# Performance work log

Hardware: AMD Instinct MI355X
Metric: run time of the kernel (lower is better)

## Reference

```python
import jax, jax.numpy as jnp
import numpy as np
from jax import lax

B, T, N, L, C, K = 8, 168, 512, 4, 32, 50

def setup_inputs() -> dict:
    key = jax.random.key(0)
    ks = iter(jax.random.split(key, 40))
    rn = lambda *s: jax.random.normal(next(ks), s, dtype=jnp.float32)
    inp = {}
    inp['input'] = rn(B, 7, T, N)
    inp['missing_nodes'] = jax.random.randint(next(ks), (B, K), 0, N)
    # two provided supports: random row-normalized adjacency
    a0 = jax.random.uniform(next(ks), (N, N)); inp['sup0'] = a0 / a0.sum(1, keepdims=True)
    a1 = jax.random.uniform(next(ks), (N, N)); inp['sup1'] = a1 / a1.sum(1, keepdims=True)
    inp['nodevec1'] = rn(N, 10); inp['nodevec2'] = rn(10, N)
    s = 0.05
    inp['skip_w'] = rn(C, 4) * s; inp['skip_b'] = jnp.zeros((C,))
    inp['filter_w'] = rn(L, C, C, 2) * s; inp['filter_b'] = jnp.zeros((L, C))
    inp['gate_w'] = rn(L, C, C, 2) * s; inp['gate_b'] = jnp.zeros((L, C))
    inp['gconv_w'] = rn(L, C, 7 * C) * s; inp['gconv_b'] = jnp.zeros((L, C))  # (2*3+1)*32=224
    inp['ingru_w'] = rn(1, C) * s; inp['ingru_b'] = jnp.zeros((1,))
    inp['regru_w'] = rn(C, 1) * s; inp['regru_b'] = jnp.zeros((C,))
    inp['zl_w'] = rn(N, 2 * N) * s; inp['zl_b'] = jnp.zeros((N,))
    inp['rl_w'] = rn(N, 2 * N) * s; inp['rl_b'] = jnp.zeros((N,))
    inp['hl_w'] = rn(N, 2 * N) * s; inp['hl_b'] = jnp.zeros((N,))
    inp['end1_w'] = rn(64, C) * s; inp['end1_b'] = jnp.zeros((64,))
    inp['end2_w'] = rn(1, 64) * s; inp['end2_b'] = jnp.zeros((1,))
    return inp

def _conv1x1(x, w, b):  # x (B,Cin,N,T), w (Cout,Cin)
    return jnp.einsum('bcnt,oc->bont', x, w) + b[None, :, None, None]

def _conv1x2(x, w, b):  # x (B,Cin,N,T+1), w (Cout,Cin,2) -> (B,Cout,N,T)
    return (jnp.einsum('bcnt,oc->bont', x[..., :-1], w[..., 0])
            + jnp.einsum('bcnt,oc->bont', x[..., 1:], w[..., 1])
            + b[None, :, None, None])

def _gcn(x, supports, w, b):  # Graph WaveNet gcn, order=2, eval mode (no dropout)
    outs = [x]
    for a in supports:
        x1 = jnp.einsum('bcnt,nm->bcmt', x, a)
        outs.append(x1)
        outs.append(jnp.einsum('bcnt,nm->bcmt', x1, a))
    return _conv1x1(jnp.concatenate(outs, axis=1), w, b)

def reference(input, missing_nodes, sup0, sup1, nodevec1, nodevec2,
              skip_w, skip_b, filter_w, filter_b, gate_w, gate_b,
              gconv_w, gconv_b, ingru_w, ingru_b, regru_w, regru_b,
              zl_w, zl_b, rl_w, rl_b, hl_w, hl_b,
              end1_w, end1_b, end2_w, end2_b):
    M = input[:, 1]                                   # (B,T,N) missingness mask
    x = jnp.transpose(input[:, jnp.array([0, 3, 5, 6])], (0, 1, 3, 2))  # (B,4,N,T)
    x = _conv1x1(x, skip_w, skip_b)                   # (B,32,N,T)
    adp = jax.nn.softmax(jax.nn.relu(nodevec1 @ nodevec2), axis=1)
    supports = [sup0, sup1, adp]
    Mt = jnp.transpose(M, (1, 0, 2))                  # (T,B,N)

    def cell(h, xm):
        Xi, Mi = xm
        xin = jax.nn.sigmoid(Xi * Mi + h * (1.0 - Mi))
        xh = jnp.concatenate([xin, h], axis=1)        # (B,2N)
        z = jax.nn.sigmoid(xh @ zl_w.T + zl_b)
        r = jax.nn.sigmoid(xh @ rl_w.T + rl_b)
        cr = jnp.concatenate([xin, r * h], axis=1)
        h_t = jnp.tanh(cr @ hl_w.T + hl_b)
        h = (1.0 - z) * h + z * h_t
        return h, h

    skip = None
    for i in range(L):
        xp = jnp.pad(x, ((0, 0), (0, 0), (0, 0), (1, 0)))    # pad time left
        residual = xp
        f = jnp.tanh(_conv1x2(xp, filter_w[i], filter_b[i]))
        g = jax.nn.sigmoid(_conv1x2(xp, gate_w[i], gate_b[i]))
        xg = f * g                                           # (B,32,N,T)
        skip = xg if skip is None else xg + skip
        gout = _gcn(xg, supports, gconv_w[i], gconv_b[i])    # (B,32,N,T); gnn == gconv output (eval)
        X = _conv1x1(gout, ingru_w, ingru_b)[:, 0]           # (B,N,T)
        Xt = jnp.transpose(X, (2, 0, 1))                     # (T,B,N)
        h0 = jnp.zeros((input.shape[0], X.shape[1]), dtype=x.dtype)
        _, outs = lax.scan(cell, h0, (Xt, Mt))               # (T,B,N)
        outputs = jnp.transpose(outs, (1, 0, 2))             # (B,T,N)
        re = _conv1x1(outputs[:, None], regru_w, regru_b)    # (B,32,T,N)
        re = jnp.transpose(re, (0, 1, 3, 2))                 # (B,32,N,T)
        x = re + residual[..., -f.shape[3]:] + gout

    h = jax.nn.relu(skip)
    h = jax.nn.relu(_conv1x1(h, end1_w, end1_b))
    h = _conv1x1(h, end2_w, end2_b)[:, 0]                    # (B,N,T)
    idx = jnp.broadcast_to(missing_nodes[:, :, None], (h.shape[0], missing_nodes.shape[1], h.shape[2]))
    return jnp.take_along_axis(h, idx, axis=1)               # (B,K,T)
```

## Files before the change

### kernel.cpp

```cpp
#include <hip/hip_runtime.h>
#include <math.h>

#define Bb 8
#define Tt 168
#define Nn 512
#define Cc 32
#define Ll 4
#define Kk 50
#define NCH 4
#define BPC 2
#define BTc (BPC*Tt)
#define BTNc ((size_t)BTc*Nn)
#define BTCNc ((size_t)BTc*Cc*Nn)
#define BT (Bb*Tt)
#define BTN ((size_t)Bb*Tt*Nn)
#define BTCN ((size_t)Bb*Tt*Cc*Nn)
#define GRUB 64

typedef __attribute__((ext_vector_type(8))) short short8v;
typedef __attribute__((ext_vector_type(4))) float f32x4;
typedef __attribute__((ext_vector_type(2))) float f32x2;

__device__ __forceinline__ float sigm(float v) { return 1.0f/(1.0f + expf(-v)); }

__device__ __forceinline__ unsigned int f2bf(float x) {
  unsigned int u = __float_as_uint(x);
  u = u + 0x7FFFu + ((u >> 16) & 1u);
  return u >> 16;
}
__device__ __forceinline__ float bf2f(unsigned int h) {
  return __uint_as_float(h << 16);
}

__device__ __forceinline__ void sysstore(float* p, float v) {
  __hip_atomic_store(p, v, __ATOMIC_RELAXED, __HIP_MEMORY_SCOPE_SYSTEM);
}
__device__ __forceinline__ int flagload(const int* p) {
  return __hip_atomic_load(p, __ATOMIC_RELAXED, __HIP_MEMORY_SCOPE_AGENT);
}
__device__ __forceinline__ void flagstore(int* p, int v) {
  __hip_atomic_store(p, v, __ATOMIC_RELAXED, __HIP_MEMORY_SCOPE_AGENT);
}

__device__ __forceinline__ void byp_store4(float* p, f32x4 v) {
  asm volatile("global_store_dwordx4 %0, %1, off sc0 sc1" :: "v"(p), "v"(v) : "memory");
}

__global__ void k_wt2(const float* __restrict__ zl, const float* __restrict__ rl,
                      const float* __restrict__ hl, float* __restrict__ wpack) {
  int idx = blockIdx.x*256 + threadIdx.x;
  if (idx >= GRUB*8*3072) return;
  int kk = idx % 3072;
  int c  = (idx / 3072) & 7;
  int sl = idx / (3072*8);
  int ncol = sl*8 + c;
  float v;
  if (kk < 1024)      v = zl[ncol*1024 + kk];
  else if (kk < 2048) v = rl[ncol*1024 + (kk-1024)];
  else if (kk < 2560) v = hl[ncol*1024 + (kk-2048)];
  else                v = hl[ncol*1024 + 512 + (kk-2560)];
  wpack[idx] = v;
}

__global__ void k_adp(const float* __restrict__ nv1, const float* __restrict__ nv2,
                      float* __restrict__ adp) {
  int i = blockIdx.x;
  __shared__ float row[512];
  __shared__ float red[256];
  float v1[10];
  #pragma unroll
  for (int k=0;k<10;k++) v1[k] = nv1[i*10+k];
  for (int jj = threadIdx.x; jj < 512; jj += 256) {
    float s = 0.f;
    #pragma unroll
    for (int k=0;k<10;k++) s += v1[k]*nv2[k*Nn + jj];
    row[jj] = fmaxf(s, 0.f);
  }
  __syncthreads();
  float m = fmaxf(row[threadIdx.x], row[threadIdx.x+256]);
  red[threadIdx.x] = m; __syncthreads();
  for (int s=128; s>0; s>>=1) { if (threadIdx.x < s) red[threadIdx.x] = fmaxf(red[threadIdx.x], red[threadIdx.x+s]); __syncthreads(); }
  float mx = red[0]; __syncthreads();
  float e0 = expf(row[threadIdx.x]      - mx);
  float e1 = expf(row[threadIdx.x+256]  - mx);
  red[threadIdx.x] = e0 + e1; __syncthreads();
  for (int s=128; s>0; s>>=1) { if (threadIdx.x < s) red[threadIdx.x] += red[threadIdx.x+s]; __syncthreads(); }
  float inv = 1.f/red[0];
  adp[(size_t)i*Nn + threadIdx.x]       = e0*inv;
  adp[(size_t)i*Nn + threadIdx.x + 256] = e1*inv;
}

__global__ void k_sprep(const float* __restrict__ S0, const float* __restrict__ S1,
                        const float* __restrict__ S2,
                        unsigned short* __restrict__ ShiT, unsigned short* __restrict__ SloT) {
  int idx = blockIdx.x*256 + threadIdx.x;
  if (idx >= 3*512*512) return;
  int s = idx >> 18;
  int rem = idx & 262143;
  int n = rem >> 9, k = rem & 511;
  const float* S = (s==0) ? S0 : (s==1) ? S1 : S2;
  float v = S[k*512 + n];
  unsigned int h = f2bf(v);
  float lo = v - bf2f(h);
  ShiT[idx] = (unsigned short)h;
  SloT[idx] = (unsigned short)f2bf(lo);
}

__launch_bounds__(256)
__global__ void k_aa(const float* __restrict__ sup0, const float* __restrict__ sup1,
                     const float* __restrict__ adp,
                     const unsigned short* __restrict__ ShiT6,
                     const unsigned short* __restrict__ SloT6,
                     float* __restrict__ A2) {
  __shared__ unsigned char smem[64*132*4];
  unsigned short* sXhi = (unsigned short*)smem;
  unsigned short* sXlo = sXhi + 2560;
  unsigned short* sShi = sXlo + 2560;
  unsigned short* sSlo = sShi + 5120;
  float* sY = (float*)smem;
#define MW 40
  const int tid  = threadIdx.x;
  const int bx   = blockIdx.x;
  const int s    = bx >> 5;
  const int r    = bx & 31;
  const int row0 = (r >> 2) * 64;
  const int n0   = (r & 3) * 128;
  const int lane = tid & 63, wv = tid >> 6;
  const int kb   = (lane >> 4)*8;
  const float* A = (s==0) ? sup0 : (s==1) ? sup1 : adp;
  const unsigned short* Shi = ShiT6 + (size_t)s*262144;
  const unsigned short* Slo = SloT6 + (size_t)s*262144;

  f32x4 acc[4][2];
  #pragma unroll
  for (int i=0;i<4;i++)
    #pragma unroll
    for (int j=0;j<2;j++) acc[i][j] = (f32x4){0.f,0.f,0.f,0.f};

  const int sm  = tid >> 2;
  const int skp = (tid & 3)*8;
  const size_t arow = (size_t)(row0 + sm)*512;
  const int sn  = tid >> 1;
  const int shp = (tid & 1)*16;

  for (int kc = 0; kc < 16; kc++) {
    const int k0 = kc*32;
    {
      float4 a0 = *reinterpret_cast<const float4*>(&A[arow + k0 + skp]);
      float4 a1 = *reinterpret_cast<const float4*>(&A[arow + k0 + skp + 4]);
      float v[8] = {a0.x,a0.y,a0.z,a0.w,a1.x,a1.y,a1.z,a1.w};
      unsigned int h[8], l[8];
      #pragma unroll
      for (int i=0;i<8;i++) { h[i] = f2bf(v[i]); l[i] = f2bf(v[i] - bf2f(h[i])); }
      uint4 H = { h[0]|(h[1]<<16), h[2]|(h[3]<<16), h[4]|(h[5]<<16), h[6]|(h[7]<<16) };
      uint4 L = { l[0]|(l[1]<<16), l[2]|(l[3]<<16), l[4]|(l[5]<<16), l[6]|(l[7]<<16) };
      *reinterpret_cast<uint4*>(&sXhi[sm*MW + skp]) = H;
      *reinterpret_cast<uint4*>(&sXlo[sm*MW + skp]) = L;
    }
    {
      const size_t srow = (size_t)(n0 + sn)*512 + k0 + shp;
      *reinterpret_cast<uint4*>(&sShi[sn*MW + shp])     = *reinterpret_cast<const uint4*>(&Shi[srow]);
      *reinterpret_cast<uint4*>(&sShi[sn*MW + shp + 8]) = *reinterpret_cast<const uint4*>(&Shi[srow + 8]);
      *reinterpret_cast<uint4*>(&sSlo[sn*MW + shp])     = *reinterpret_cast<const uint4*>(&Slo[srow]);
      *reinterpret_cast<uint4*>(&sSlo[sn*MW + shp + 8]) = *reinterpret_cast<const uint4*>(&Slo[srow + 8]);
    }
    __syncthreads();
    short8v bhi[2], blo[2];
    #pragma unroll
    for (int ct=0; ct<2; ct++) {
      int col = wv*32 + ct*16 + (lane & 15);
      bhi[ct] = *reinterpret_cast<const short8v*>(&sShi[col*MW + kb]);
      blo[ct] = *reinterpret_cast<const short8v*>(&sSlo[col*MW + kb]);
    }
    #pragma unroll
    for (int rt=0; rt<4; rt++) {
      int row = rt*16 + (lane & 15);
      short8v ahi = *reinterpret_cast<const short8v*>(&sXhi[row*MW + kb]);
      short8v alo = *reinterpret_cast<const short8v*>(&sXlo[row*MW + kb]);
      #pragma unroll
      for (int ct=0; ct<2; ct++) {
        acc[rt][ct] = __builtin_amdgcn_mfma_f32_16x16x32_bf16(ahi, bhi[ct], acc[rt][ct], 0, 0, 0);
        acc[rt][ct] = __builtin_amdgcn_mfma_f32_16x16x32_bf16(ahi, blo[ct], acc[rt][ct], 0, 0, 0);
        acc[rt][ct] = __builtin_amdgcn_mfma_f32_16x16x32_bf16(alo, bhi[ct], acc[rt][ct], 0, 0, 0);
      }
    }
    __syncthreads();
  }
  #pragma unroll
  for (int rt=0; rt<4; rt++) {
    #pragma unroll
    for (int ct=0; ct<2; ct++) {
      int col = wv*32 + ct*16 + (lane & 15);
      int rbase = rt*16 + (lane >> 4)*4;
      sY[(rbase+0)*132 + col] = acc[rt][ct].x;
      sY[(rbase+1)*132 + col] = acc[rt][ct].y;
      sY[(rbase+2)*132 + col] = acc[rt][ct].z;
      sY[(rbase+3)*132 + col] = acc[rt][ct].w;
    }
  }
  __syncthreads();
  for (int e = tid; e < 2048; e += 256) {
    int m = e >> 5, c4 = (e & 31)*4;
    float4 v = *reinterpret_cast<const float4*>(&sY[m*132 + c4]);
    *reinterpret_cast<float4*>(&A2[(size_t)s*262144 + (size_t)(row0 + m)*512 + n0 + c4]) = v;
  }
#undef MW
}

__global__ void k_intransform(const float* __restrict__ input, const float* __restrict__ skw,
                              const float* __restrict__ skb, float* __restrict__ x) {
  size_t idx = (size_t)blockIdx.x*256 + threadIdx.x;
  if (idx >= BTN) return;
  int n = idx & 511;
  size_t bt = idx >> 9;
  int b = (int)(bt / Tt), t = (int)(bt % Tt);
  size_t chs = (size_t)Tt*Nn;
  size_t base = (((size_t)b*7)*Tt + t)*Nn + n;
  float v0 = input[base + 0*chs];
  float v3 = input[base + 3*chs];
  float v5 = input[base + 5*chs];
  float v6 = input[base + 6*chs];
  float* xp = x + bt*Cc*Nn + n;
  #pragma unroll
  for (int c=0;c<32;c++)
    xp[(size_t)c*Nn] = skb[c] + skw[c*4+0]*v0 + skw[c*4+1]*v3 + skw[c*4+2]*v5 + skw[c*4+3]*v6;
}

__launch_bounds__(256)
__global__ void k_fgconv(const float* __restrict__ x, const float* __restrict__ fw,
                         const float* __restrict__ fb, const float* __restrict__ gw,
                         const float* __restrict__ gb, const float* __restrict__ gcwl,
                         const float* __restrict__ gcb,
                         float* __restrict__ xg, float* __restrict__ gout,
                         int chunk, int wgout) {
  __shared__ float sfw[2048], sgw[2048], sw0[1024], sfb[32], sgb[32], sgcb[32];
  for (int l = threadIdx.x; l < 2048; l += 256) { sfw[l] = fw[l]; sgw[l] = gw[l]; }
  for (int l = threadIdx.x; l < 1024; l += 256) sw0[l] = gcwl[(l>>5)*224 + (l&31)];
  if (threadIdx.x < 32) {
    sfb[threadIdx.x] = fb[threadIdx.x];
    sgb[threadIdx.x] = gb[threadIdx.x];
    sgcb[threadIdx.x] = gcb[threadIdx.x];
  }
  __syncthreads();
  size_t idx = (size_t)blockIdx.x*256 + threadIdx.x;
  if (idx >= BTNc) return;
  int n = idx & 511;
  size_t btl = idx >> 9;
  int t = (int)(btl % Tt);
  size_t btg = (size_t)chunk*BTc + btl;
  const float* xp = x + btg*Cc*Nn + n;
  float xl[32], xr[32];
  #pragma unroll
  for (int c=0;c<32;c++) xr[c] = xp[(size_t)c*Nn];
  if (t == 0) {
    #pragma unroll
    for (int c=0;c<32;c++) xl[c] = 0.f;
  } else {
    const float* xq = xp - (size_t)Cc*Nn;
    #pragma unroll
    for (int c=0;c<32;c++) xl[c] = xq[(size_t)c*Nn];
  }
  float xgv[32];
  for (int c=0;c<32;c++) {
    float f = sfb[c], g = sgb[c];
    #pragma unroll
    for (int cp=0;cp<32;cp++) {
      f += xl[cp]*sfw[(c*32+cp)*2] + xr[cp]*sfw[(c*32+cp)*2+1];
      g += xl[cp]*sgw[(c*32+cp)*2] + xr[cp]*sgw[(c*32+cp)*2+1];
    }
    xgv[c] = tanhf(f) * sigm(g);
  }
  float* xgp = xg + btl*Cc*Nn + n;
  #pragma unroll
  for (int c=0;c<32;c++) xgp[(size_t)c*Nn] = xgv[c];
  if (wgout) {
    float* gp = gout + btl*Cc*Nn + n;
    for (int o=0;o<32;o++) {
      float s = sgcb[o];
      #pragma unroll
      for (int c=0;c<32;c++) s += sw0[o*32+c]*xgv[c];
      gp[(size_t)o*Nn] = s;
    }
  }
}

__launch_bounds__(256, 3)
__global__ void k_supall2(const float* __restrict__ X,
                          const unsigned short* __restrict__ ShiT6,
                          const unsigned short* __restrict__ SloT6,
                          const float* __restrict__ gcw,
                          float* __restrict__ gout) {
  __shared__ __align__(16) unsigned char smem[64*132*4];
  __shared__ float sWp[1024];
  unsigned short* sXhi = (unsigned short*)smem;
  unsigned short* sXlo = sXhi + 2560;
  unsigned short* sShi = sXlo + 2560;
  unsigned short* sSlo = sShi + 5120;
  float* sY = (float*)smem;
#define MW 40
  const int tid  = threadIdx.x;
  const int bt2  = blockIdx.x >> 2;
  const int colg = blockIdx.x & 3;
  const int bt0  = bt2*2;
  const int n0   = colg*128;
  const int lane = tid & 63, wv = tid >> 6;
  const int kb   = (lane >> 4)*8;
  const int sm   = tid >> 2;
  const int skp  = (tid & 3)*8;
  const size_t xrow = ((size_t)(bt0 + (sm>>5))*Cc + (sm&31))*Nn;
  const int sn   = tid >> 1;
  const int shp  = (tid & 1)*16;
  const int tx = tid & 31, ty = tid >> 5;

  float og[2][4][4];
  #pragma unroll
  for (int bl=0;bl<2;bl++)
    #pragma unroll
    for (int i=0;i<4;i++)
      #pragma unroll
      for (int j=0;j<4;j++) og[bl][i][j] = 0.f;

  for (int p = 0; p < 6; p++) {
    const int s = p >> 1, j = p & 1;
    const int panel = j ? (3 + s) : s;
    const unsigned short* Shi = ShiT6 + (size_t)panel*262144;
    const unsigned short* Slo = SloT6 + (size_t)panel*262144;

    __syncthreads();
    for (int l = tid; l < 1024; l += 256)
      sWp[l] = gcw[(l>>5)*224 + (p+1)*32 + (l&31)];
    {
      float4 a0 = *reinterpret_cast<const float4*>(&X[xrow + skp]);
      float4 a1 = *reinterpret_cast<const float4*>(&X[xrow + skp + 4]);
      float v[8] = {a0.x,a0.y,a0.z,a0.w,a1.x,a1.y,a1.z,a1.w};
      unsigned int h[8], l[8];
      #pragma unroll
      for (int i=0;i<8;i++) { h[i] = f2bf(v[i]); l[i] = f2bf(v[i] - bf2f(h[i])); }
      uint4 H = { h[0]|(h[1]<<16), h[2]|(h[3]<<16), h[4]|(h[5]<<16), h[6]|(h[7]<<16) };
      uint4 L = { l[0]|(l[1]<<16), l[2]|(l[3]<<16), l[4]|(l[5]<<16), l[6]|(l[7]<<16) };
      *reinterpret_cast<uint4*>(&sXhi[sm*MW + skp]) = H;
      *reinterpret_cast<uint4*>(&sXlo[sm*MW + skp]) = L;
      const size_t srow = (size_t)(n0 + sn)*512 + shp;
      *reinterpret_cast<uint4*>(&sShi[sn*MW + shp])     = *reinterpret_cast<const uint4*>(&Shi[srow]);
      *reinterpret_cast<uint4*>(&sShi[sn*MW + shp + 8]) = *reinterpret_cast<const uint4*>(&Shi[srow + 8]);
      *reinterpret_cast<uint4*>(&sSlo[sn*MW + shp])     = *reinterpret_cast<const uint4*>(&Slo[srow]);
      *reinterpret_cast<uint4*>(&sSlo[sn*MW + shp + 8]) = *reinterpret_cast<const uint4*>(&Slo[srow + 8]);
    }
    __syncthreads();

    f32x4 acc[4][2];
    #pragma unroll
    for (int i=0;i<4;i++)
      #pragma unroll
      for (int jj=0;jj<2;jj++) acc[i][jj] = (f32x4){0.f,0.f,0.f,0.f};

    for (int kc = 0; kc < 16; kc++) {
      float4 pa0, pa1; uint4 ps0, ps1, ps2, ps3;
      if (kc < 15) {
        const int k1 = (kc+1)*32;
        pa0 = *reinterpret_cast<const float4*>(&X[xrow + k1 + skp]);
        pa1 = *reinterpret_cast<const float4*>(&X[xrow + k1 + skp + 4]);
        const size_t srow = (size_t)(n0 + sn)*512 + k1 + shp;
        ps0 = *reinterpret_cast<const uint4*>(&Shi[srow]);
        ps1 = *reinterpret_cast<const uint4*>(&Shi[srow + 8]);
        ps2 = *reinterpret_cast<const uint4*>(&Slo[srow]);
        ps3 = *reinterpret_cast<const uint4*>(&Slo[srow + 8]);
      }
      short8v bhi[2], blo[2];
      #pragma unroll
      for (int ct=0; ct<2; ct++) {
        int col = wv*32 + ct*16 + (lane & 15);
        bhi[ct] = *reinterpret_cast<const short8v*>(&sShi[col*MW + kb]);
        blo[ct] = *reinterpret_cast<const short8v*>(&sSlo[col*MW + kb]);
      }
      #pragma unroll
      for (int rt=0; rt<4; rt++) {
        int row = rt*16 + (lane & 15);
        short8v ahi = *reinterpret_cast<const short8v*>(&sXhi[row*MW + kb]);
        short8v alo = *reinterpret_cast<const short8v*>(&sXlo[row*MW + kb]);
        #pragma unroll
        for (int ct=0; ct<2; ct++) {
          acc[rt][ct] = __builtin_amdgcn_mfma_f32_16x16x32_bf16(ahi, bhi[ct], acc[rt][ct], 0, 0, 0);
          acc[rt][ct] = __builtin_amdgcn_mfma_f32_16x16x32_bf16(ahi, blo[ct], acc[rt][ct], 0, 0, 0);
          acc[rt][ct] = __builtin_amdgcn_mfma_f32_16x16x32_bf16(alo, bhi[ct], acc[rt][ct], 0, 0, 0);
        }
      }
      __syncthreads();
      if (kc < 15) {
        float v[8] = {pa0.x,pa0.y,pa0.z,pa0.w,pa1.x,pa1.y,pa1.z,pa1.w};
        unsigned int h[8], l[8];
        #pragma unroll
        for (int i=0;i<8;i++) { h[i] = f2bf(v[i]); l[i] = f2bf(v[i] - bf2f(h[i])); }
        uint4 H = { h[0]|(h[1]<<16), h[2]|(h[3]<<16), h[4]|(h[5]<<16), h[6]|(h[7]<<16) };
        uint4 L = { l[0]|(l[1]<<16), l[2]|(l[3]<<16), l[4]|(l[5]<<16), l[6]|(l[7]<<16) };
        *reinterpret_cast<uint4*>(&sXhi[sm*MW + skp]) = H;
        *reinterpret_cast<uint4*>(&sXlo[sm*MW + skp]) = L;
        *reinterpret_cast<uint4*>(&sShi[sn*MW + shp])     = ps0;
        *reinterpret_cast<uint4*>(&sShi[sn*MW + shp + 8]) = ps1;
        *reinterpret_cast<uint4*>(&sSlo[sn*MW + shp])     = ps2;
        *reinterpret_cast<uint4*>(&sSlo[sn*MW + shp + 8]) = ps3;
      }
      __syncthreads();
    }
    #pragma unroll
    for (int rt=0; rt<4; rt++) {
      #pragma unroll
      for (int ct=0; ct<2; ct++) {
        int col = wv*32 + ct*16 + (lane & 15);
        int rbase = rt*16 + (lane >> 4)*4;
        sY[(rbase+0)*132 + col] = acc[rt][ct].x;
        sY[(rbase+1)*132 + col] = acc[rt][ct].y;
        sY[(rbase+2)*132 + col] = acc[rt][ct].z;
        sY[(rbase+3)*132 + col] = acc[rt][ct].w;
      }
    }
    __syncthreads();
    for (int btl = 0; btl < 2; btl++) {
      #pragma unroll 8
      for (int c = 0; c < 32; c++) {
        float4 yv = *reinterpret_cast<const float4*>(&sY[(btl*32 + c)*132 + tx*4]);
        float w0 = sWp[((ty<<2)+0)*32 + c];
        float w1 = sWp[((ty<<2)+1)*32 + c];
        float w2 = sWp[((ty<<2)+2)*32 + c];
        float w3 = sWp[((ty<<2)+3)*32 + c];
        og[btl][0][0]+=w0*yv.x; og[btl][0][1]+=w0*yv.y; og[btl][0][2]+=w0*yv.z; og[btl][0][3]+=w0*yv.w;
        og[btl][1][0]+=w1*yv.x; og[btl][1][1]+=w1*yv.y; og[btl][1][2]+=w1*yv.z; og[btl][1][3]+=w1*yv.w;
        og[btl][2][0]+=w2*yv.x; og[btl][2][1]+=w2*yv.y; og[btl][2][2]+=w2*yv.z; og[btl][2][3]+=w2*yv.w;
        og[btl][3][0]+=w3*yv.x; og[btl][3][1]+=w3*yv.y; og[btl][3][2]+=w3*yv.z; og[btl][3][3]+=w3*yv.w;
      }
    }
  }
  for (int btl = 0; btl < 2; btl++) {
    float* gp = gout + (size_t)(bt0+btl)*Cc*Nn + n0 + (tx<<2);
    #pragma unroll
    for (int i=0;i<4;i++) {
      float4 cur = *reinterpret_cast<float4*>(gp + (size_t)((ty<<2)+i)*Nn);
      cur.x += og[btl][i][0]; cur.y += og[btl][i][1]; cur.z += og[btl][i][2]; cur.w += og[btl][i][3];
      *reinterpret_cast<float4*>(gp + (size_t)((ty<<2)+i)*Nn) = cur;
    }
  }
#undef MW
}

__global__ void k_skipgather(const float* __restrict__ xg, const int* __restrict__ miss,
                             float* __restrict__ skipK, int chunk, int first) {
  int idx = blockIdx.x*256 + threadIdx.x;
  if (idx >= BPC*Kk*Tt) return;
  int t = idx % Tt;
  int k = (idx / Tt) % Kk;
  int bloc = idx / (Tt*Kk);
  int bg = chunk*BPC + bloc;
  int node = miss[bg*Kk + k];
  const float* xp = xg + (((size_t)bloc*Tt + t)*Cc)*Nn + node;
  float* sp = skipK + (((size_t)bg*Kk + k)*Cc)*Tt + t;
  #pragma unroll
  for (int c=0;c<32;c++) {
    float v = xp[(size_t)c*Nn];
    sp[(size_t)c*Tt] = first ? v : (sp[(size_t)c*Tt] + v);
  }
}

__global__ void k_ingruxf(const float* __restrict__ gout, const float* __restrict__ iw,
                          const float* __restrict__ ib2, float* __restrict__ Xs,
                          float* __restrict__ x, int chunk) {
  size_t idx = (size_t)blockIdx.x*256 + threadIdx.x;
  if (idx >= BTNc) return;
  int n = idx & 511;
  size_t btl = idx >> 9;
  int b = chunk*BPC + (int)(btl / Tt), t = (int)(btl % Tt);
  const float* gp = gout + btl*Cc*Nn + n;
  float* xp = x + ((size_t)chunk*BTc + btl)*Cc*Nn + n;
  float s = ib2[0];
  #pragma unroll
  for (int c=0;c<Cc;c++) {
    float g = gp[(size_t)c*Nn];
    s += iw[c]*g;
    xp[(size_t)c*Nn] += g;
  }
  Xs[((size_t)t*Bb + b)*Nn + n] = s;
}

__launch_bounds__(512, 1)
__global__ void k_gru7(const float* __restrict__ Xs, const float* __restrict__ input,
                       const float* __restrict__ wpack,
                       const float* __restrict__ zb, const float* __restrict__ rb,
                       const float* __restrict__ hb,
                       float* __restrict__ xh_g, float* __restrict__ rh_g,
                       float* __restrict__ outs, int* __restrict__ flags) {
  __shared__ float wl[8*3072];
  const int tid = threadIdx.x;
  const int sl  = blockIdx.x;
  const int n0  = sl*8;
  const int b   = tid >> 6;
  const int q   = tid & 63;

  {
    const float4* src = reinterpret_cast<const float4*>(wpack + (size_t)sl*24576);
    float4* dst = reinterpret_cast<float4*>(wl);
    #pragma unroll 4
    for (int i = tid; i < 6144; i += 512) dst[i] = src[i];
  }
  if (q < 8) {
    int nn = n0 + q;
    float Xi = Xs[(size_t)b*Nn + nn];
    float Mi = input[(((size_t)b*7+1)*Tt + 0)*Nn + nn];
    sysstore(xh_g + b*1024 + 512 + nn, 0.f);
    sysstore(xh_g + b*1024 + nn, sigm(Xi*Mi));
  }
  __syncthreads();
  asm volatile("s_waitcnt vmcnt(0)" ::: "memory");
  if (q == 0) flagstore(flags + (b*64 + sl)*32, 1);

  const int* pollfl = flags + (b*64 + q)*32;
  int* myfl = flags + (b*64 + sl)*32;

  float zbv[8], rbv[8], hbv[8];
  #pragma unroll
  for (int c=0;c<8;c++) { zbv[c]=zb[n0+c]; rbv[c]=rb[n0+c]; hbv[c]=hb[n0+c]; }

  const float* bp = xh_g + b*1024;
  const float* rp = rh_g + b*512;

  for (int t = 0; t < Tt; t++) {
    float4 xiA, xiB, miA, miB;
    {
      int tp = (t+1 < Tt) ? (t+1) : t;
      const float* xsp = Xs + ((size_t)tp*Bb + b)*Nn + n0;
      const float* mip = input + (((size_t)b*7+1)*Tt + tp)*Nn + n0;
      xiA = *reinterpret_cast<const float4*>(xsp);
      xiB = *reinterpret_cast<const float4*>(xsp + 4);
      miA = *reinterpret_cast<const float4*>(mip);
      miB = *reinterpret_cast<const float4*>(mip + 4);
    }
    {
      int tgt = 1 + 2*t;
      while (!__all(flagload(pollfl) >= tgt)) __builtin_amdgcn_s_sleep(1);
    }
    f32x2 xv[8]; f32x4 h0v, h1v;
    asm volatile(
      "global_load_dwordx2 %0, %10, off sc0 sc1\n\t"
      "global_load_dwordx2 %1, %11, off sc0 sc1\n\t"
      "global_load_dwordx2 %2, %12, off sc0 sc1\n\t"
      "global_load_dwordx2 %3, %13, off sc0 sc1\n\t"
      "global_load_dwordx2 %4, %14, off sc0 sc1\n\t"
      "global_load_dwordx2 %5, %15, off sc0 sc1\n\t"
      "global_load_dwordx2 %6, %16, off sc0 sc1\n\t"
      "global_load_dwordx2 %7, %17, off sc0 sc1\n\t"
      "global_load_dwordx4 %8, %18, off sc0 sc1\n\t"
      "global_load_dwordx4 %9, %19, off sc0 sc1\n\t"
      "s_waitcnt vmcnt(0)"
      : "=&v"(xv[0]), "=&v"(xv[1]), "=&v"(xv[2]), "=&v"(xv[3]),
        "=&v"(xv[4]), "=&v"(xv[5]), "=&v"(xv[6]), "=&v"(xv[7]),
        "=&v"(h0v), "=&v"(h1v)
      : "v"(bp + 0*128 + q*2), "v"(bp + 1*128 + q*2), "v"(bp + 2*128 + q*2), "v"(bp + 3*128 + q*2),
        "v"(bp + 4*128 + q*2), "v"(bp + 5*128 + q*2), "v"(bp + 6*128 + q*2), "v"(bp + 7*128 + q*2),
        "v"(bp + 512 + n0), "v"(bp + 512 + n0 + 4)
      : "memory");
    float hold[8] = {h0v.x, h0v.y, h0v.z, h0v.w, h1v.x, h1v.y, h1v.z, h1v.w};
    float az[8], ar[8], ax[8];
    #pragma unroll
    for (int c=0;c<8;c++) { az[c]=0.f; ar[c]=0.f; ax[c]=0.f; }
    #pragma unroll
    for (int i = 0; i < 8; i++) {
      int k = i*128 + q*2;
      #pragma unroll
      for (int c = 0; c < 8; c++) {
        float2 wz = *reinterpret_cast<const float2*>(wl + c*3072 + k);
        float2 wr = *reinterpret_cast<const float2*>(wl + c*3072 + 1024 + k);
        az[c] += xv[i].x*wz.x + xv[i].y*wz.y;
        ar[c] += xv[i].x*wr.x + xv[i].y*wr.y;
      }
    }
    #pragma unroll
    for (int i = 0; i < 4; i++) {
      int k = i*128 + q*2;
      #pragma unroll
      for (int c = 0; c < 8; c++) {
        float2 wx = *reinterpret_cast<const float2*>(wl + c*3072 + 2048 + k);
        ax[c] += xv[i].x*wx.x + xv[i].y*wx.y;
      }
    }
    #pragma unroll
    for (int d = 1; d < 64; d <<= 1) {
      #pragma unroll
      for (int c = 0; c < 8; c++) {
        az[c] += __shfl_xor(az[c], d);
        ar[c] += __shfl_xor(ar[c], d);
        ax[c] += __shfl_xor(ax[c], d);
      }
    }
    float zs[8], rh[8];
    #pragma unroll
    for (int c = 0; c < 8; c++) {
      zs[c] = sigm(az[c] + zbv[c]);
      float r = sigm(ar[c] + rbv[c]);
      rh[c] = r * hold[c];
    }
    if (q == 0) {
      f32x4 r0 = {rh[0],rh[1],rh[2],rh[3]};
      f32x4 r1 = {rh[4],rh[5],rh[6],rh[7]};
      byp_store4(rh_g + b*512 + n0,     r0);
      byp_store4(rh_g + b*512 + n0 + 4, r1);
      asm volatile("s_waitcnt vmcnt(0)" ::: "memory");
      flagstore(myfl, 2 + 2*t);
    }
    {
      int tgt = 2 + 2*t;
      while (!__all(flagload(pollfl) >= tgt)) __builtin_amdgcn_s_sleep(1);
    }
    f32x2 rv[4];
    asm volatile(
      "global_load_dwordx2 %0, %4, off sc0 sc1\n\t"
      "global_load_dwordx2 %1, %5, off sc0 sc1\n\t"
      "global_load_dwordx2 %2, %6, off sc0 sc1\n\t"
      "global_load_dwordx2 %3, %7, off sc0 sc1\n\t"
      "s_waitcnt vmcnt(0)"
      : "=&v"(rv[0]), "=&v"(rv[1]), "=&v"(rv[2]), "=&v"(rv[3])
      : "v"(rp + 0*128 + q*2), "v"(rp + 1*128 + q*2), "v"(rp + 2*128 + q*2), "v"(rp + 3*128 + q*2)
      : "memory");
    float ah[8];
    #pragma unroll
    for (int c=0;c<8;c++) ah[c]=0.f;
    #pragma unroll
    for (int i = 0; i < 4; i++) {
      int k = i*128 + q*2;
      #pragma unroll
      for (int c = 0; c < 8; c++) {
        float2 wh = *reinterpret_cast<const float2*>(wl + c*3072 + 2560 + k);
        ah[c] += rv[i].x*wh.x + rv[i].y*wh.y;
      }
    }
    #pragma unroll
    for (int d = 1; d < 64; d <<= 1) {
      #pragma unroll
      for (int c = 0; c < 8; c++) ah[c] += __shfl_xor(ah[c], d);
    }
    float hn[8];
    #pragma unroll
    for (int c = 0; c < 8; c++) {
      float ht = tanhf(ax[c] + ah[c] + hbv[c]);
      hn[c] = (1.f - zs[c])*hold[c] + zs[c]*ht;
    }
    if (q == 0) {
      f32x4 h0 = {hn[0],hn[1],hn[2],hn[3]};
      f32x4 h1 = {hn[4],hn[5],hn[6],hn[7]};
      *reinterpret_cast<f32x4*>(&outs[((size_t)t*Bb + b)*Nn + n0])     = h0;
      *reinterpret_cast<f32x4*>(&outs[((size_t)t*Bb + b)*Nn + n0 + 4]) = h1;
      byp_store4(xh_g + b*1024 + 512 + n0,     h0);
      byp_store4(xh_g + b*1024 + 512 + n0 + 4, h1);
      if (t+1 < Tt) {
        f32x4 x0, x1;
        x0.x = sigm(xiA.x*miA.x + hn[0]*(1.f - miA.x));
        x0.y = sigm(xiA.y*miA.y + hn[1]*(1.f - miA.y));
        x0.z = sigm(xiA.z*miA.z + hn[2]*(1.f - miA.z));
        x0.w = sigm(xiA.w*miA.w + hn[3]*(1.f - miA.w));
        x1.x = sigm(xiB.x*miB.x + hn[4]*(1.f - miB.x));
        x1.y = sigm(xiB.y*miB.y + hn[5]*(1.f - miB.y));
        x1.z = sigm(xiB.z*miB.z + hn[6]*(1.f - miB.z));
        x1.w = sigm(xiB.w*miB.w + hn[7]*(1.f - miB.w));
        byp_store4(xh_g + b*1024 + n0,     x0);
        byp_store4(xh_g + b*1024 + n0 + 4, x1);
      }
      asm volatile("s_waitcnt vmcnt(0)" ::: "memory");
      flagstore(myfl, 3 + 2*t);
    }
  }
}

__global__ void k_xre(float* __restrict__ x, const float* __restrict__ outs,
                      const float* __restrict__ rw, const float* __restrict__ rb2) {
  size_t idx = (size_t)blockIdx.x*256 + threadIdx.x;
  if (idx >= BTCN) return;
  int n = idx & 511;
  int c = (int)((idx >> 9) & 31);
  size_t bt = idx >> 14;
  int b = (int)(bt / Tt), t = (int)(bt % Tt);
  float o = outs[((size_t)t*Bb + b)*Nn + n];
  x[idx] += o*rw[c] + rb2[c];
}

__launch_bounds__(256)
__global__ void k_head(const float* __restrict__ skipK,
                       const float* __restrict__ e1w, const float* __restrict__ e1b,
                       const float* __restrict__ e2w, const float* __restrict__ e2b,
                       float* __restrict__ out) {
  __shared__ float sw[2048], sb[64], s2[64];
  for (int l = threadIdx.x; l < 2048; l += 256) sw[l] = e1w[l];
  if (threadIdx.x < 64) { sb[threadIdx.x] = e1b[threadIdx.x]; s2[threadIdx.x] = e2w[threadIdx.x]; }
  __syncthreads();
  int idx = blockIdx.x*256 + threadIdx.x;
  if (idx >= Bb*Kk*Tt) return;
  int t = idx % Tt;
  int k = (idx / Tt) % Kk;
  int b = idx / (Tt*Kk);
  const float* sp = skipK + (((size_t)b*Kk + k)*Cc)*Tt + t;
  float in[32];
  #pragma unroll
  for (int c=0;c<32;c++) in[c] = fmaxf(sp[(size_t)c*Tt], 0.f);
  float acc = e2b[0];
  for (int o=0;o<64;o++) {
    float s = sb[o];
    #pragma unroll
    for (int c=0;c<32;c++) s += sw[o*32+c]*in[c];
    acc += s2[o]*fmaxf(s, 0.f);
  }
  out[idx] = acc;
}

extern "C" void kernel_launch(void* const* d_in, const int* in_sizes, int n_in,
                              void* d_out, int out_size, void* d_ws, size_t ws_size,
                              hipStream_t stream) {
  const float* input = (const float*)d_in[0];
  const int*   miss  = (const int*)  d_in[1];
  const float* sup0  = (const float*)d_in[2];
  const float* sup1  = (const float*)d_in[3];
  const float* nv1   = (const float*)d_in[4];
  const float* nv2   = (const float*)d_in[5];
  const float* skw   = (const float*)d_in[6];
  const float* skb   = (const float*)d_in[7];
  const float* fw    = (const float*)d_in[8];
  const float* fb    = (const float*)d_in[9];
  const float* gw    = (const float*)d_in[10];
  const float* gb    = (const float*)d_in[11];
  const float* gcw   = (const float*)d_in[12];
  const float* gcb   = (const float*)d_in[13];
  const float* iw    = (const float*)d_in[14];
  const float* ib2   = (const float*)d_in[15];
  const float* rw    = (const float*)d_in[16];
  const float* rb2   = (const float*)d_in[17];
  const float* zl    = (const float*)d_in[18];
  const float* zb    = (const float*)d_in[19];
  const float* rl    = (const float*)d_in[20];
  const float* rb    = (const float*)d_in[21];
  const float* hl    = (const float*)d_in[22];
  const float* hb    = (const float*)d_in[23];
  const float* e1w   = (const float*)d_in[24];
  const float* e1b   = (const float*)d_in[25];
  const float* e2w   = (const float*)d_in[26];
  const float* e2b   = (const float*)d_in[27];
  float* out = (float*)d_out;

  float* p     = (float*)d_ws;
  float* x     = p; p += BTCN;
  float* xg    = p; p += BTCNc;
  float* gout  = p; p += BTCNc;
  float* skipK = p; p += (size_t)Bb*Kk*Cc*Tt;
  float* adp   = p; p += (size_t)Nn*Nn;
  float* A2    = p; p += (size_t)3*Nn*Nn;
  float* wpack = p; p += (size_t)GRUB*8*3072;
  unsigned short* ShiT6 = (unsigned short*)p; p += (size_t)(6*512*512)/2;
  unsigned short* SloT6 = (unsigned short*)p; p += (size_t)(6*512*512)/2;
  float* Xs    = p; p += (size_t)Tt*Bb*Nn;
  float* outs  = p; p += (size_t)Tt*Bb*Nn;
  float* xh_g  = p; p += Bb*1024;
  float* rh_g  = p; p += Bb*512;
  int*   flags = (int*)p; p += (size_t)Bb*GRUB*32;

  k_wt2<<<(GRUB*8*3072 + 255)/256, 256, 0, stream>>>(zl, rl, hl, wpack);
  k_adp<<<Nn, 256, 0, stream>>>(nv1, nv2, adp);
  k_sprep<<<(3*512*512 + 255)/256, 256, 0, stream>>>(sup0, sup1, adp, ShiT6, SloT6);
  k_aa<<<96, 256, 0, stream>>>(sup0, sup1, adp, ShiT6, SloT6, A2);
  k_sprep<<<(3*512*512 + 255)/256, 256, 0, stream>>>(A2, A2 + 262144, A2 + 524288,
                                                     ShiT6 + 3*262144, SloT6 + 3*262144);
  k_intransform<<<(int)((BTN + 255)/256), 256, 0, stream>>>(input, skw, skb, x);

  for (int layer = 0; layer < Ll; layer++) {
    const int last = (layer == Ll - 1);
    for (int chunk = 0; chunk < NCH; chunk++) {
      k_fgconv<<<(int)((BTNc + 255)/256), 256, 0, stream>>>(
          x, fw + layer*2048, fb + layer*32, gw + layer*2048, gb + layer*32,
          gcw + layer*32*224, gcb + layer*32,
          xg, gout, chunk, last ? 0 : 1);
      if (!last) {
        k_supall2<<<dim3((BTc/2)*4), 256, 0, stream>>>(
            xg, ShiT6, SloT6, gcw + layer*32*224, gout);
      }
      k_skipgather<<<(BPC*Kk*Tt + 255)/256, 256, 0, stream>>>(xg, miss, skipK, chunk, layer == 0 ? 1 : 0);
      if (!last) {
        k_ingruxf<<<(int)((BTNc + 255)/256), 256, 0, stream>>>(gout, iw, ib2, Xs, x, chunk);
      }
    }
    if (!last) {
      (void)hipMemsetAsync(flags, 0, (size_t)Bb*GRUB*32*sizeof(int), stream);
      k_gru7<<<dim3(GRUB), dim3(512), 0, stream>>>(
          Xs, input, wpack, zb, rb, hb, xh_g, rh_g, outs, flags);
      k_xre<<<(int)((BTCN + 255)/256), 256, 0, stream>>>(x, outs, rw, rb2);
    }
  }
  k_head<<<(Bb*Kk*Tt + 255)/256, 256, 0, stream>>>(skipK, e1w, e1b, e2w, e2b, out);
}
```

Before: 11.00 ms.

## Fuse skip gather into filter/gate kernel and in-GRU projection into support GEMM epilogue

The missing-node skip accumulation moves into the filter/gate kernel: each thread checks whether its node is in the block's missing list and writes its 32 gated channels straight to skipK. The in-GRU 1x1 projection and residual add move into the support-GEMM epilogue, which reduces across warps through shared memory. This drops two kernel launches per chunk and a full re-read of gout and xg. It adds a 50-iteration compare loop per thread, and the last layer no longer writes xg at all.

Measured after the change: 10.83 ms. About the same (-1.6%).

```diff
diff --git a/kernel.cpp b/kernel.cpp
--- a/kernel.cpp
+++ b/kernel.cpp
@@ -227,13 +227,20 @@
 }
 
 __launch_bounds__(256)
-__global__ void k_fgconv(const float* __restrict__ x, const float* __restrict__ fw,
-                         const float* __restrict__ fb, const float* __restrict__ gw,
-                         const float* __restrict__ gb, const float* __restrict__ gcwl,
-                         const float* __restrict__ gcb,
-                         float* __restrict__ xg, float* __restrict__ gout,
-                         int chunk, int wgout) {
+__global__ void k_fgconv2(const float* __restrict__ x, const float* __restrict__ fw,
+                          const float* __restrict__ fb, const float* __restrict__ gw,
+                          const float* __restrict__ gb, const float* __restrict__ gcwl,
+                          const float* __restrict__ gcb,
+                          const int* __restrict__ miss, float* __restrict__ skipK,
+                          float* __restrict__ xg, float* __restrict__ gout,
+                          int chunk, int wxg, int first) {
   __shared__ float sfw[2048], sgw[2048], sw0[1024], sfb[32], sgb[32], sgcb[32];
+  __shared__ int smiss[Kk];
+  size_t idx = (size_t)blockIdx.x*256 + threadIdx.x;
+  int n = idx & 511;
+  size_t btl = idx >> 9;
+  int t = (int)(btl % Tt);
+  int bg = chunk*BPC + (int)(btl / Tt);
   for (int l = threadIdx.x; l < 2048; l += 256) { sfw[l] = fw[l]; sgw[l] = gw[l]; }
   for (int l = threadIdx.x; l < 1024; l += 256) sw0[l] = gcwl[(l>>5)*224 + (l&31)];
   if (threadIdx.x < 32) {
@@ -241,14 +248,9 @@
     sgb[threadIdx.x] = gb[threadIdx.x];
     sgcb[threadIdx.x] = gcb[threadIdx.x];
   }
+  if (threadIdx.x < Kk) smiss[threadIdx.x] = miss[bg*Kk + threadIdx.x];
   __syncthreads();
-  size_t idx = (size_t)blockIdx.x*256 + threadIdx.x;
-  if (idx >= BTNc) return;
-  int n = idx & 511;
-  size_t btl = idx >> 9;
-  int t = (int)(btl % Tt);
-  size_t btg = (size_t)chunk*BTc + btl;
-  const float* xp = x + btg*Cc*Nn + n;
+  const float* xp = x + ((size_t)chunk*BTc + btl)*Cc*Nn + n;
   float xl[32], xr[32];
   #pragma unroll
   for (int c=0;c<32;c++) xr[c] = xp[(size_t)c*Nn];
@@ -270,10 +272,10 @@
     }
     xgv[c] = tanhf(f) * sigm(g);
   }
-  float* xgp = xg + btl*Cc*Nn + n;
-  #pragma unroll
-  for (int c=0;c<32;c++) xgp[(size_t)c*Nn] = xgv[c];
-  if (wgout) {
+  if (wxg) {
+    float* xgp = xg + btl*Cc*Nn + n;
+    #pragma unroll
+    for (int c=0;c<32;c++) xgp[(size_t)c*Nn] = xgv[c];
     float* gp = gout + btl*Cc*Nn + n;
     for (int o=0;o<32;o++) {
       float s = sgcb[o];
@@ -282,16 +284,31 @@
       gp[(size_t)o*Nn] = s;
     }
   }
+  for (int k = 0; k < Kk; k++) {
+    if (smiss[k] == n) {
+      float* sp = skipK + (((size_t)bg*Kk + k)*Cc)*Tt + t;
+      if (first) {
+        #pragma unroll
+        for (int c=0;c<32;c++) sp[(size_t)c*Tt] = xgv[c];
+      } else {
+        #pragma unroll
+        for (int c=0;c<32;c++) sp[(size_t)c*Tt] += xgv[c];
+      }
+    }
+  }
 }
 
 __launch_bounds__(256, 3)
-__global__ void k_supall2(const float* __restrict__ X,
+__global__ void k_supall3(const float* __restrict__ X,
                           const unsigned short* __restrict__ ShiT6,
                           const unsigned short* __restrict__ SloT6,
                           const float* __restrict__ gcw,
-                          float* __restrict__ gout) {
+                          const float* __restrict__ gout,
+                          const float* __restrict__ iw, const float* __restrict__ ib2,
+                          float* __restrict__ x, float* __restrict__ Xs, int chunk) {
   __shared__ __align__(16) unsigned char smem[64*132*4];
   __shared__ float sWp[1024];
+  __shared__ float siw[32];
   unsigned short* sXhi = (unsigned short*)smem;
   unsigned short* sXlo = sXhi + 2560;
   unsigned short* sShi = sXlo + 2560;
@@ -312,6 +329,8 @@
   const int shp  = (tid & 1)*16;
   const int tx = tid & 31, ty = tid >> 5;
 
+  if (tid < 32) siw[tid] = iw[tid];
+
   float og[2][4][4];
   #pragma unroll
   for (int bl=0;bl<2;bl++)
@@ -430,54 +449,37 @@
       }
     }
   }
+  __syncthreads();
+  float* sRed = (float*)smem;
+  const float ib = ib2[0];
   for (int btl = 0; btl < 2; btl++) {
-    float* gp = gout + (size_t)(bt0+btl)*Cc*Nn + n0 + (tx<<2);
+    const int btg = bt0 + btl;
+    const float* gp = gout + (size_t)btg*Cc*Nn + n0 + (tx<<2);
+    float* xp = x + ((size_t)chunk*BTc + btg)*Cc*Nn + n0 + (tx<<2);
+    float part[4] = {0.f, 0.f, 0.f, 0.f};
     #pragma unroll
     for (int i=0;i<4;i++) {
-      float4 cur = *reinterpret_cast<float4*>(gp + (size_t)((ty<<2)+i)*Nn);
+      float4 cur = *reinterpret_cast<const float4*>(gp + (size_t)((ty<<2)+i)*Nn);
       cur.x += og[btl][i][0]; cur.y += og[btl][i][1]; cur.z += og[btl][i][2]; cur.w += og[btl][i][3];
-      *reinterpret_cast<float4*>(gp + (size_t)((ty<<2)+i)*Nn) = cur;
-    }
+      float4 xv = *reinterpret_cast<const float4*>(xp + (size_t)((ty<<2)+i)*Nn);
+      xv.x += cur.x; xv.y += cur.y; xv.z += cur.z; xv.w += cur.w;
+      *reinterpret_cast<float4*>(xp + (size_t)((ty<<2)+i)*Nn) = xv;
+      float w = siw[(ty<<2)+i];
+      part[0] += w*cur.x; part[1] += w*cur.y; part[2] += w*cur.z; part[3] += w*cur.w;
+    }
+    *reinterpret_cast<float4*>(&sRed[ty*128 + (tx<<2)]) =
+        make_float4(part[0], part[1], part[2], part[3]);
+    __syncthreads();
+    if (tid < 128) {
+      float s = ib;
+      #pragma unroll
+      for (int g = 0; g < 8; g++) s += sRed[g*128 + tid];
+      int b = chunk*BPC + btg/Tt, t = btg % Tt;
+      Xs[((size_t)t*Bb + b)*Nn + n0 + tid] = s;
+    }
+    __syncthreads();
   }
 #undef MW
-}
-
-__global__ void k_skipgather(const float* __restrict__ xg, const int* __restrict__ miss,
-                             float* __restrict__ skipK, int chunk, int first) {
-  int idx = blockIdx.x*256 + threadIdx.x;
-  if (idx >= BPC*Kk*Tt) return;
-  int t = idx % Tt;
-  int k = (idx / Tt) % Kk;
-  int bloc = idx / (Tt*Kk);
-  int bg = chunk*BPC + bloc;
-  int node = miss[bg*Kk + k];
-  const float* xp = xg + (((size_t)bloc*Tt + t)*Cc)*Nn + node;
-  float* sp = skipK + (((size_t)bg*Kk + k)*Cc)*Tt + t;
-  #pragma unroll
-  for (int c=0;c<32;c++) {
-    float v = xp[(size_t)c*Nn];
-    sp[(size_t)c*Tt] = first ? v : (sp[(size_t)c*Tt] + v);
-  }
-}
-
-__global__ void k_ingruxf(const float* __restrict__ gout, const float* __restrict__ iw,
-                          const float* __restrict__ ib2, float* __restrict__ Xs,
-                          float* __restrict__ x, int chunk) {
-  size_t idx = (size_t)blockIdx.x*256 + threadIdx.x;
-  if (idx >= BTNc) return;
-  int n = idx & 511;
-  size_t btl = idx >> 9;
-  int b = chunk*BPC + (int)(btl / Tt), t = (int)(btl % Tt);
-  const float* gp = gout + btl*Cc*Nn + n;
-  float* xp = x + ((size_t)chunk*BTc + btl)*Cc*Nn + n;
-  float s = ib2[0];
-  #pragma unroll
-  for (int c=0;c<Cc;c++) {
-    float g = gp[(size_t)c*Nn];
-    s += iw[c]*g;
-    xp[(size_t)c*Nn] += g;
-  }
-  Xs[((size_t)t*Bb + b)*Nn + n] = s;
 }
 
 __launch_bounds__(512, 1)
@@ -767,17 +769,13 @@
   for (int layer = 0; layer < Ll; layer++) {
     const int last = (layer == Ll - 1);
     for (int chunk = 0; chunk < NCH; chunk++) {
-      k_fgconv<<<(int)((BTNc + 255)/256), 256, 0, stream>>>(
+      k_fgconv2<<<(int)((BTNc + 255)/256), 256, 0, stream>>>(
           x, fw + layer*2048, fb + layer*32, gw + layer*2048, gb + layer*32,
           gcw + layer*32*224, gcb + layer*32,
-          xg, gout, chunk, last ? 0 : 1);
+          miss, skipK, xg, gout, chunk, last ? 0 : 1, layer == 0 ? 1 : 0);
       if (!last) {
-        k_supall2<<<dim3((BTc/2)*4), 256, 0, stream>>>(
-            xg, ShiT6, SloT6, gcw + layer*32*224, gout);
-      }
-      k_skipgather<<<(BPC*Kk*Tt + 255)/256, 256, 0, stream>>>(xg, miss, skipK, chunk, layer == 0 ? 1 : 0);
-      if (!last) {
-        k_ingruxf<<<(int)((BTNc + 255)/256), 256, 0, stream>>>(gout, iw, ib2, Xs, x, chunk);
+        k_supall3<<<dim3((BTc/2)*4), 256, 0, stream>>>(
+            xg, ShiT6, SloT6, gcw + layer*32*224, gout, iw, ib2, x, Xs, chunk);
       }
     }
     if (!last) {
```
